# Performance work log

Measured on AMD Instinct MI355X. Metric: run time of the kernel, lower is better.

The kernel has to match this reference:

```python
import jax, jax.numpy as jnp
import numpy as np

ALIGN_SCALE = 3.0
UNIF_SCALE = 1.0
EPS = 1e-12  # torch F.normalize eps


def _normalize(x):
    n = jnp.linalg.norm(x, axis=-1, keepdims=True)
    return x / jnp.maximum(n, EPS)


def _unif_loss(a, b):
    # log(mean(exp(-2 * ||a_i - b_j||^2))) over all N*M pairs, fused via GEMM identity
    sq_a = jnp.sum(a * a, axis=1)  # [N]
    sq_b = jnp.sum(b * b, axis=1)  # [M]
    # squared distances: ||a||^2 + ||b||^2 - 2 a.b, clipped at 0 for numerics
    d2 = jnp.maximum(sq_a[:, None] + sq_b[None, :] - 2.0 * (a @ b.T), 0.0)  # [N, M]
    return jnp.log(jnp.mean(jnp.exp(-2.0 * d2)))


def setup_inputs() -> dict:
    key = jax.random.key(0)
    k1, k2 = jax.random.split(key)
    N, D = 8192, 512
    return {
        "image_embed": jax.random.normal(k1, (N, D), dtype=jnp.float32),
        "text_embed": jax.random.normal(k2, (N, D), dtype=jnp.float32),
    }


def reference(image_embed, text_embed):
    img = _normalize(image_embed)
    txt = _normalize(text_embed)
    # alignment: mean squared L2 between paired embeddings
    diff = img - txt
    align_loss = jnp.mean(jnp.sum(diff * diff, axis=1))
    # single device: gathered-all tensors equal the local tensors
    text_unif = _unif_loss(txt, txt)
    image_unif = _unif_loss(img, img)
    unif_loss = (text_unif + image_unif) / 2.0
    return ALIGN_SCALE * align_loss + UNIF_SCALE * unif_loss
```

## Files before the change

### kernel.cpp

```cpp
#include <hip/hip_runtime.h>
#include <hip/hip_bf16.h>


#define NROWS 8192
#define DBYTES 512
#define NT    64
#define NTILES 2080
#define SCALE_SPLAT 0x75757575

typedef __attribute__((ext_vector_type(8)))  int   int8v;
typedef __attribute__((ext_vector_type(4)))  int   int4v;
typedef __attribute__((ext_vector_type(16))) float float16v;

__device__ inline void load_lds16(const void* g, void* l) {
    __builtin_amdgcn_global_load_lds(
        (const __attribute__((address_space(1))) void*)g,
        (__attribute__((address_space(3))) void*)l, 16, 0, 0);
}

__global__ __launch_bounds__(256) void normalize_kernel(
    const float* __restrict__ img, const float* __restrict__ txt,
    unsigned char* __restrict__ nimg, unsigned char* __restrict__ ntxt,
    float* __restrict__ alignp)
{
    const int lane = threadIdx.x & 63;
    const int wave = threadIdx.x >> 6;
    const int row  = blockIdx.x * 4 + wave;

    const float4* pi = (const float4*)(img + (size_t)row * 512);
    const float4* pt = (const float4*)(txt + (size_t)row * 512);
    const float4 i0 = pi[lane], i1 = pi[lane + 64];
    const float4 t0 = pt[lane], t1 = pt[lane + 64];

    float ssi = i0.x*i0.x + i0.y*i0.y + i0.z*i0.z + i0.w*i0.w
              + i1.x*i1.x + i1.y*i1.y + i1.z*i1.z + i1.w*i1.w;
    float sst = t0.x*t0.x + t0.y*t0.y + t0.z*t0.z + t0.w*t0.w
              + t1.x*t1.x + t1.y*t1.y + t1.z*t1.z + t1.w*t1.w;
    float dot = i0.x*t0.x + i0.y*t0.y + i0.z*t0.z + i0.w*t0.w
              + i1.x*t1.x + i1.y*t1.y + i1.z*t1.z + i1.w*t1.w;

    #pragma unroll
    for (int off = 1; off < 64; off <<= 1) {
        ssi += __shfl_xor(ssi, off);
        sst += __shfl_xor(sst, off);
        dot += __shfl_xor(dot, off);
    }
    const float inv_i = 1.0f / fmaxf(sqrtf(ssi), 1e-12f);
    const float inv_t = 1.0f / fmaxf(sqrtf(sst), 1e-12f);
    const float si = 1024.0f * inv_i;
    const float st = 1024.0f * inv_t;

    int p0 = __builtin_amdgcn_cvt_pk_fp8_f32(i0.x*si, i0.y*si, 0, false);
    p0     = __builtin_amdgcn_cvt_pk_fp8_f32(i0.z*si, i0.w*si, p0, true);
    int p1 = __builtin_amdgcn_cvt_pk_fp8_f32(i1.x*si, i1.y*si, 0, false);
    p1     = __builtin_amdgcn_cvt_pk_fp8_f32(i1.z*si, i1.w*si, p1, true);
    int q0 = __builtin_amdgcn_cvt_pk_fp8_f32(t0.x*st, t0.y*st, 0, false);
    q0     = __builtin_amdgcn_cvt_pk_fp8_f32(t0.z*st, t0.w*st, q0, true);
    int q1 = __builtin_amdgcn_cvt_pk_fp8_f32(t1.x*st, t1.y*st, 0, false);
    q1     = __builtin_amdgcn_cvt_pk_fp8_f32(t1.z*st, t1.w*st, q1, true);

    int* oi = (int*)(nimg + (size_t)row * DBYTES);
    int* ot = (int*)(ntxt + (size_t)row * DBYTES);
    oi[lane] = p0; oi[lane + 64] = p1;
    ot[lane] = q0; ot[lane + 64] = q1;

    __shared__ float r4[4];
    if (lane == 0) r4[wave] = dot * inv_i * inv_t;
    __syncthreads();
    if (threadIdx.x == 0)
        alignp[blockIdx.x] = r4[0] + r4[1] + r4[2] + r4[3];
}

__global__ __launch_bounds__(256) void gram_kernel(
    const unsigned char* __restrict__ A0,
    const unsigned char* __restrict__ A1,
    float* __restrict__ S)
{
    const int t = blockIdx.x;
    int i = (int)((129.0f - sqrtf(129.0f * 129.0f - 8.0f * (float)t)) * 0.5f);
    while ((i + 1) * (129 - (i + 1)) / 2 <= t) ++i;
    while (i * (129 - i) / 2 > t) --i;
    const int j = i + (t - i * (129 - i) / 2);

    const unsigned char* __restrict__ A = blockIdx.y ? A1 : A0;
    const int tid  = threadIdx.x;
    const int lane = tid & 63;
    const int wave = tid >> 6;
    const int wm = wave & 1, wn = wave >> 1;
    const int lr = lane & 31;
    const int h  = lane >> 5;

    const unsigned char* gA = A + (size_t)i * 128 * DBYTES;
    const unsigned char* gB = A + (size_t)j * 128 * DBYTES;

    __shared__ __align__(16) unsigned char ldsA[128 * 128];
    __shared__ __align__(16) unsigned char ldsB[128 * 128];

    float16v acc[2][2];
    #pragma unroll
    for (int a = 0; a < 2; ++a)
        #pragma unroll
        for (int b = 0; b < 2; ++b)
            #pragma unroll
            for (int r = 0; r < 16; ++r) acc[a][b][r] = 0.0f;

    for (int k0 = 0; k0 < DBYTES; k0 += 128) {
        #pragma unroll
        for (int rnd = 0; rnd < 4; ++rnd) {
            const int slot = rnd * 4096 + tid * 16;
            const int r    = slot >> 7;
            const int cp   = (slot >> 4) & 7;
            const int cl   = cp ^ (r & 7);
            load_lds16(gA + (size_t)r * DBYTES + k0 + cl * 16, &ldsA[slot]);
            load_lds16(gB + (size_t)r * DBYTES + k0 + cl * 16, &ldsB[slot]);
        }
        __syncthreads();

        #pragma unroll
        for (int kk = 0; kk < 2; ++kk) {
            const int cbase = kk * 4 + h * 2;
            int8v av[2], bv[2];
            #pragma unroll
            for (int mt = 0; mt < 2; ++mt) {
                const int r = wm * 64 + mt * 32 + lr;
                const int4v q0 = *(const int4v*)&ldsA[r * 128 + ((cbase    ) ^ (r & 7)) * 16];
                const int4v q1 = *(const int4v*)&ldsA[r * 128 + ((cbase + 1) ^ (r & 7)) * 16];
                av[mt][0]=q0[0]; av[mt][1]=q0[1]; av[mt][2]=q0[2]; av[mt][3]=q0[3];
                av[mt][4]=q1[0]; av[mt][5]=q1[1]; av[mt][6]=q1[2]; av[mt][7]=q1[3];
            }
            #pragma unroll
            for (int nt = 0; nt < 2; ++nt) {
                const int r = wn * 64 + nt * 32 + lr;
                const int4v q0 = *(const int4v*)&ldsB[r * 128 + ((cbase    ) ^ (r & 7)) * 16];
                const int4v q1 = *(const int4v*)&ldsB[r * 128 + ((cbase + 1) ^ (r & 7)) * 16];
                bv[nt][0]=q0[0]; bv[nt][1]=q0[1]; bv[nt][2]=q0[2]; bv[nt][3]=q0[3];
                bv[nt][4]=q1[0]; bv[nt][5]=q1[1]; bv[nt][6]=q1[2]; bv[nt][7]=q1[3];
            }
            #pragma unroll
            for (int mt = 0; mt < 2; ++mt)
                #pragma unroll
                for (int nt = 0; nt < 2; ++nt)
                    acc[mt][nt] = __builtin_amdgcn_mfma_scale_f32_32x32x64_f8f6f4(
                        av[mt], bv[nt], acc[mt][nt],
                        0, 0,
                        0, SCALE_SPLAT,
                        0, SCALE_SPLAT);
        }
        __syncthreads();
    }

    float s = 0.0f;
    #pragma unroll
    for (int mt = 0; mt < 2; ++mt)
        #pragma unroll
        for (int nt = 0; nt < 2; ++nt)
            #pragma unroll
            for (int r2 = 0; r2 < 16; ++r2) {
                const float g = acc[mt][nt][r2];
                s += __expf(4.0f * fminf(g, 1.0f) - 4.0f);
            }
    #pragma unroll
    for (int off = 32; off; off >>= 1) s += __shfl_down(s, off);
    __shared__ float ps[4];
    if (lane == 0) ps[wave] = s;
    __syncthreads();
    if (tid == 0) {
        const float tot = ps[0] + ps[1] + ps[2] + ps[3];
        const float w = (i == j) ? 1.0f : 2.0f;
        atomicAdd(&S[blockIdx.y * 32 + (blockIdx.x & 31)], tot * w);
    }
}

__global__ __launch_bounds__(256) void finalize_kernel(
    const float* __restrict__ S,
    const float* __restrict__ alignp,
    float* __restrict__ out)
{
    const int tid = threadIdx.x;
    float a = 0.0f;
    #pragma unroll
    for (int k = 0; k < 8; ++k) a += alignp[tid + 256 * k];
    #pragma unroll
    for (int off = 32; off; off >>= 1) a += __shfl_down(a, off);
    __shared__ float r4[4];
    if ((tid & 63) == 0) r4[tid >> 6] = a;
    __syncthreads();
    if (tid == 0) {
        const double A = (double)r4[0] + r4[1] + r4[2] + r4[3];
        double si = 0.0, st = 0.0;
        for (int k = 0; k < 32; ++k) { si += S[k]; st += S[32 + k]; }
        const double align = 2.0 - 2.0 * A / (double)NROWS;
        const double n2 = (double)NROWS * (double)NROWS;
        const double unif = 0.5 * (log(si / n2) + log(st / n2));
        out[0] = (float)(3.0 * align + unif);
    }
}

extern "C" void kernel_launch(void* const* d_in, const int* in_sizes, int n_in,
                              void* d_out, int out_size, void* d_ws, size_t ws_size,
                              hipStream_t stream) {
    const float* img = (const float*)d_in[0];
    const float* txt = (const float*)d_in[1];
    char* ws = (char*)d_ws;
    unsigned char* nimg = (unsigned char*)ws;
    unsigned char* ntxt = (unsigned char*)(ws + (size_t)NROWS * DBYTES);
    float* S      = (float*)(ws + 2 * (size_t)NROWS * DBYTES);
    float* alignp = S + 64;

    hipMemsetAsync(S, 0, 64 * sizeof(float), stream);
    normalize_kernel<<<NROWS / 4, 256, 0, stream>>>(img, txt, nimg, ntxt, alignp);
    dim3 grid(NTILES, 2);
    gram_kernel<<<grid, 256, 0, stream>>>(nimg, ntxt, S);
    finalize_kernel<<<1, 256, 0, stream>>>(S, alignp, (float*)d_out);
}
```

Measured before the change: 129.2 us.

## Fuse finalize into gram kernel via last-block counter and change LDS swizzle

Result: slower. 192.7 us (+49.2%).

```diff
diff --git a/kernel.cpp b/kernel.cpp
--- a/kernel.cpp
+++ b/kernel.cpp
@@ -6,6 +6,7 @@
 #define DBYTES 512
 #define NT    64
 #define NTILES 2080
+#define NBLOCKS_TOTAL (NTILES * 2)
 #define SCALE_SPLAT 0x75757575
 
 typedef __attribute__((ext_vector_type(8)))  int   int8v;
@@ -17,6 +18,8 @@
         (const __attribute__((address_space(1))) void*)g,
         (__attribute__((address_space(3))) void*)l, 16, 0, 0);
 }
+
+__device__ inline int swz(int r) { return (r ^ (r >> 3)) & 7; }
 
 __global__ __launch_bounds__(256) void normalize_kernel(
     const float* __restrict__ img, const float* __restrict__ txt,
@@ -74,7 +77,10 @@
 __global__ __launch_bounds__(256) void gram_kernel(
     const unsigned char* __restrict__ A0,
     const unsigned char* __restrict__ A1,
-    float* __restrict__ S)
+    float* __restrict__ S,
+    int* __restrict__ done,
+    const float* __restrict__ alignp,
+    float* __restrict__ out)
 {
     const int t = blockIdx.x;
     int i = (int)((129.0f - sqrtf(129.0f * 129.0f - 8.0f * (float)t)) * 0.5f);
@@ -110,7 +116,7 @@
             const int slot = rnd * 4096 + tid * 16;
             const int r    = slot >> 7;
             const int cp   = (slot >> 4) & 7;
-            const int cl   = cp ^ (r & 7);
+            const int cl   = cp ^ swz(r);
             load_lds16(gA + (size_t)r * DBYTES + k0 + cl * 16, &ldsA[slot]);
             load_lds16(gB + (size_t)r * DBYTES + k0 + cl * 16, &ldsB[slot]);
         }
@@ -123,16 +129,18 @@
             #pragma unroll
             for (int mt = 0; mt < 2; ++mt) {
                 const int r = wm * 64 + mt * 32 + lr;
-                const int4v q0 = *(const int4v*)&ldsA[r * 128 + ((cbase    ) ^ (r & 7)) * 16];
-                const int4v q1 = *(const int4v*)&ldsA[r * 128 + ((cbase + 1) ^ (r & 7)) * 16];
+                const int s = swz(r);
+                const int4v q0 = *(const int4v*)&ldsA[r * 128 + ((cbase    ) ^ s) * 16];
+                const int4v q1 = *(const int4v*)&ldsA[r * 128 + ((cbase + 1) ^ s) * 16];
                 av[mt][0]=q0[0]; av[mt][1]=q0[1]; av[mt][2]=q0[2]; av[mt][3]=q0[3];
                 av[mt][4]=q1[0]; av[mt][5]=q1[1]; av[mt][6]=q1[2]; av[mt][7]=q1[3];
             }
             #pragma unroll
             for (int nt = 0; nt < 2; ++nt) {
                 const int r = wn * 64 + nt * 32 + lr;
-                const int4v q0 = *(const int4v*)&ldsB[r * 128 + ((cbase    ) ^ (r & 7)) * 16];
-                const int4v q1 = *(const int4v*)&ldsB[r * 128 + ((cbase + 1) ^ (r & 7)) * 16];
+                const int s = swz(r);
+                const int4v q0 = *(const int4v*)&ldsB[r * 128 + ((cbase    ) ^ s) * 16];
+                const int4v q1 = *(const int4v*)&ldsB[r * 128 + ((cbase + 1) ^ s) * 16];
                 bv[nt][0]=q0[0]; bv[nt][1]=q0[1]; bv[nt][2]=q0[2]; bv[nt][3]=q0[3];
                 bv[nt][4]=q1[0]; bv[nt][5]=q1[1]; bv[nt][6]=q1[2]; bv[nt][7]=q1[3];
             }
@@ -162,37 +170,38 @@
     #pragma unroll
     for (int off = 32; off; off >>= 1) s += __shfl_down(s, off);
     __shared__ float ps[4];
+    __shared__ int is_last;
     if (lane == 0) ps[wave] = s;
     __syncthreads();
     if (tid == 0) {
         const float tot = ps[0] + ps[1] + ps[2] + ps[3];
         const float w = (i == j) ? 1.0f : 2.0f;
         atomicAdd(&S[blockIdx.y * 32 + (blockIdx.x & 31)], tot * w);
-    }
-}
-
-__global__ __launch_bounds__(256) void finalize_kernel(
-    const float* __restrict__ S,
-    const float* __restrict__ alignp,
-    float* __restrict__ out)
-{
-    const int tid = threadIdx.x;
-    float a = 0.0f;
-    #pragma unroll
-    for (int k = 0; k < 8; ++k) a += alignp[tid + 256 * k];
-    #pragma unroll
-    for (int off = 32; off; off >>= 1) a += __shfl_down(a, off);
-    __shared__ float r4[4];
-    if ((tid & 63) == 0) r4[tid >> 6] = a;
+        __threadfence();
+        const int old = atomicAdd(done, 1);
+        is_last = (old == NBLOCKS_TOTAL - 1) ? 1 : 0;
+    }
     __syncthreads();
-    if (tid == 0) {
-        const double A = (double)r4[0] + r4[1] + r4[2] + r4[3];
-        double si = 0.0, st = 0.0;
-        for (int k = 0; k < 32; ++k) { si += S[k]; st += S[32 + k]; }
-        const double align = 2.0 - 2.0 * A / (double)NROWS;
-        const double n2 = (double)NROWS * (double)NROWS;
-        const double unif = 0.5 * (log(si / n2) + log(st / n2));
-        out[0] = (float)(3.0 * align + unif);
+
+    if (is_last && wave == 0) {
+        float sv = atomicAdd(&S[lane], 0.0f);
+        #pragma unroll
+        for (int off = 1; off < 32; off <<= 1) sv += __shfl_xor(sv, off);
+        const float s_img = __shfl(sv, 0);
+        const float s_txt = __shfl(sv, 32);
+
+        float a = 0.0f;
+        #pragma unroll
+        for (int k = 0; k < 32; ++k) a += alignp[lane + 64 * k];
+        #pragma unroll
+        for (int off = 1; off < 64; off <<= 1) a += __shfl_xor(a, off);
+
+        if (lane == 0) {
+            const double align = 2.0 - 2.0 * (double)a / (double)NROWS;
+            const double n2 = (double)NROWS * (double)NROWS;
+            const double unif = 0.5 * (log((double)s_img / n2) + log((double)s_txt / n2));
+            out[0] = (float)(3.0 * align + unif);
+        }
     }
 }
 
@@ -205,11 +214,11 @@
     unsigned char* nimg = (unsigned char*)ws;
     unsigned char* ntxt = (unsigned char*)(ws + (size_t)NROWS * DBYTES);
     float* S      = (float*)(ws + 2 * (size_t)NROWS * DBYTES);
-    float* alignp = S + 64;
-
-    hipMemsetAsync(S, 0, 64 * sizeof(float), stream);
+    int*   done   = (int*)(S + 64);
+    float* alignp = (float*)(done + 1);
+
+    hipMemsetAsync(S, 0, 65 * sizeof(float), stream);
     normalize_kernel<<<NROWS / 4, 256, 0, stream>>>(img, txt, nimg, ntxt, alignp);
     dim3 grid(NTILES, 2);
-    gram_kernel<<<grid, 256, 0, stream>>>(nimg, ntxt, S);
-    finalize_kernel<<<1, 256, 0, stream>>>(S, alignp, (float*)d_out);
-}
+    gram_kernel<<<grid, 256, 0, stream>>>(nimg, ntxt, S, done, alignp, (float*)d_out);
+}
```
